# Kernel optimization log

Hardware: AMD Instinct MI355X
Metric: run time of the kernel (lower is better)

The kernel has to match this reference:

```python
import jax, jax.numpy as jnp
import numpy as np

N_ITERS = 3
EPS = 1e-5


def _ln(x, g, b):
    mu = jnp.mean(x, axis=-1, keepdims=True)
    var = jnp.mean((x - mu) ** 2, axis=-1, keepdims=True)
    return (x - mu) * jax.lax.rsqrt(var + EPS) * g + b


def setup_inputs() -> dict:
    key = jax.random.key(0)
    ks = iter(jax.random.split(key, 32))
    B, N, D_in, H, K = 128, 1024, 192, 128, 3

    def lin(o, i):
        w = (jax.random.normal(next(ks), (o, i)) / np.sqrt(i)).astype(jnp.float32)
        return w, jnp.zeros((o,), jnp.float32)

    Wp, bp = lin(H, D_in)
    Wq, bq = lin(H, H)
    Wk, bk = lin(H, H)
    Wv, bv = lin(H, H)
    Wih, bih = lin(3 * H, H)   # GRUCell input weights, stacked [r, z, n]
    Whh, bhh = lin(3 * H, H)   # GRUCell hidden weights
    W1, b1 = lin(2 * H, H)     # MLP expand
    W2, b2 = lin(H, 2 * H)     # MLP project
    ones = jnp.ones((H,), jnp.float32)
    zeros = jnp.zeros((H,), jnp.float32)

    return {
        "patch_tokens": jax.random.normal(next(ks), (B, N, D_in), jnp.float32),
        "noise": jax.random.normal(next(ks), (B, K, H), jnp.float32),
        "slot_mu": (jax.random.normal(next(ks), (1, K, H)) * 0.02).astype(jnp.float32),
        "slot_log_sigma": jnp.zeros((1, K, H), jnp.float32),
        "Wp": Wp, "bp": bp, "g_in": ones, "b_in": zeros,
        "Wq": Wq, "bq": bq, "Wk": Wk, "bk": bk, "Wv": Wv, "bv": bv,
        "Wih": Wih, "bih": bih, "Whh": Whh, "bhh": bhh,
        "g_s": ones, "b_s": zeros,
        "W1": W1, "b1": b1, "W2": W2, "b2": b2,
        "g_m": ones, "b_m": zeros,
    }


def reference(patch_tokens, noise, slot_mu, slot_log_sigma,
              Wp, bp, g_in, b_in,
              Wq, bq, Wk, bk, Wv, bv,
              Wih, bih, Whh, bhh,
              g_s, b_s, W1, b1, W2, b2, g_m, b_m):
    H = slot_mu.shape[-1]
    scale = 1.0 / jnp.sqrt(jnp.asarray(H, patch_tokens.dtype))

    # project + LayerNorm inputs once (k, v depend only on inputs -> hoisted)
    inputs = _ln(patch_tokens @ Wp.T + bp, g_in, b_in)      # (B, N, H)
    k = inputs @ Wk.T + bk                                  # (B, N, H)
    v = inputs @ Wv.T + bv                                  # (B, N, H)

    slots = slot_mu + jnp.exp(slot_log_sigma) * noise       # (B, K, H)

    def gru_cell(x, h):
        gi = x @ Wih.T + bih                                # (B, K, 3H)
        gh = h @ Whh.T + bhh
        ir, iz, inn = jnp.split(gi, 3, axis=-1)
        hr, hz, hn = jnp.split(gh, 3, axis=-1)
        r = jax.nn.sigmoid(ir + hr)
        z = jax.nn.sigmoid(iz + hz)
        n = jnp.tanh(inn + r * hn)
        return (1.0 - z) * n + z * h

    attn_weights = None
    for _ in range(N_ITERS):
        slots_prev = slots
        s = _ln(slots, g_s, b_s)
        q = s @ Wq.T + bq                                   # (B, K, H)
        attn = jnp.einsum('bkd,bnd->bkn', q, k) * scale     # (B, K, N)
        attn_weights = jax.nn.softmax(attn, axis=1)         # softmax over slots
        updates = jnp.einsum('bkn,bnd->bkd', attn_weights, v)
        slots = gru_cell(updates, slots_prev)
        h = _ln(slots, g_m, b_m)
        slots = slots + (jax.nn.gelu(h @ W1.T + b1, approximate=False) @ W2.T + b2)

    return slots, attn_weights
```

## Files before the change

### kernel.cpp

```cpp
#include <hip/hip_runtime.h>
#include <math.h>

constexpr float EPS = 1e-5f;
constexpr float SCALE = 0.08838834764831845f;

using f32x4  = __attribute__((ext_vector_type(4))) float;
using bf16x8 = __attribute__((ext_vector_type(8))) short;
using us8    = __attribute__((ext_vector_type(8))) unsigned short;

__device__ __forceinline__ unsigned short f2b_rne(float f) {
    unsigned int x = __float_as_uint(f);
    return (unsigned short)((x + 0x7fffu + ((x >> 16) & 1u)) >> 16);
}

__device__ __forceinline__ int swz32(int row, int k8) {
    int f = (row & 3) ^ ((row >> 2) & 3);
    return row * 32 + ((k8 ^ f) << 3);
}

__global__ __launch_bounds__(256) void split_weights_kernel(
    const float* __restrict__ Wp, const float* __restrict__ Wk,
    const float* __restrict__ Wv, unsigned short* __restrict__ hi,
    unsigned short* __restrict__ lo)
{
    int idx = blockIdx.x * 256 + threadIdx.x;
    float v;
    if (idx < 24576)      v = Wp[idx];
    else if (idx < 40960) v = Wk[idx - 24576];
    else                  v = Wv[idx - 40960];
    unsigned int bits = __float_as_uint(v);
    hi[idx] = (unsigned short)(bits >> 16);
    lo[idx] = f2b_rne(v - __uint_as_float(bits & 0xffff0000u));
}

__global__ __launch_bounds__(256) void pack_weights_kernel(
    const float* __restrict__ Wih, const float* __restrict__ Whh,
    const float* __restrict__ W1, const float* __restrict__ W2,
    const float* __restrict__ Wq, float4* __restrict__ out)
{
    int idx = blockIdx.x * 256 + threadIdx.x;
    const float* src; int OUT, base, K;
    if (idx < 12288)      { src = Wih; OUT = 384; base = 0;     K = 128; }
    else if (idx < 24576) { src = Whh; OUT = 384; base = 12288; K = 128; }
    else if (idx < 32768) { src = W1;  OUT = 256; base = 24576; K = 128; }
    else if (idx < 40960) { src = W2;  OUT = 128; base = 32768; K = 256; }
    else                  { src = Wq;  OUT = 128; base = 40960; K = 128; }
    int li = idx - base;
    int kq = li / OUT, t = li - kq * OUT;
    float4 v;
    v.x = src[(size_t)t * K + 4 * kq];
    v.y = src[(size_t)t * K + 4 * kq + 1];
    v.z = src[(size_t)t * K + 4 * kq + 2];
    v.w = src[(size_t)t * K + 4 * kq + 3];
    out[idx] = v;
}

__global__ __launch_bounds__(256, 3) void fused_proj_kv_kernel(
    const float* __restrict__ patch,
    const unsigned short* __restrict__ Wphi, const unsigned short* __restrict__ Wplo,
    const unsigned short* __restrict__ Wkhi, const unsigned short* __restrict__ Wklo,
    const unsigned short* __restrict__ Wvhi, const unsigned short* __restrict__ Wvlo,
    const float* __restrict__ biasp, const float* __restrict__ g_in,
    const float* __restrict__ b_in, const float* __restrict__ biask,
    const float* __restrict__ biasv,
    float* __restrict__ kout, float* __restrict__ vout)
{
    __shared__ __align__(16) unsigned short mem[24576];

    const int tid  = threadIdx.x;
    const int lane = tid & 63, wave = tid >> 6;
    const int ln15 = lane & 15, quad = lane >> 4;
    const int m0   = blockIdx.x * 64;

    const int wrow = wave * 16;
    f32x4 acc1[8];
#pragma unroll
    for (int nt = 0; nt < 8; nt++)
#pragma unroll
        for (int r = 0; r < 4; r++) acc1[nt][r] = 0.f;

    const int arow = tid >> 2, ak8 = tid & 3;
    const float* aptr = patch + (size_t)(m0 + arow) * 192 + ak8 * 8;
    float4 pa0 = *(const float4*)aptr;
    float4 pa1 = *(const float4*)(aptr + 4);
    us8 pbh[2], pbl[2];
    int boff[2];
#pragma unroll
    for (int i = 0; i < 2; i++) {
        int c = tid + 256 * i;
        boff[i] = (c >> 2) * 192 + (c & 3) * 8;
        pbh[i] = *(const us8*)(Wphi + boff[i]);
        pbl[i] = *(const us8*)(Wplo + boff[i]);
    }

    const int ea = swz32(wrow + ln15, quad);

    for (int kk = 0; kk < 192; kk += 32) {
        {
            float va[8] = {pa0.x, pa0.y, pa0.z, pa0.w, pa1.x, pa1.y, pa1.z, pa1.w};
            us8 h, l;
#pragma unroll
            for (int j = 0; j < 8; j++) {
                unsigned int bits = __float_as_uint(va[j]);
                h[j] = (unsigned short)(bits >> 16);
                l[j] = f2b_rne(va[j] - __uint_as_float(bits & 0xffff0000u));
            }
            int e = swz32(arow, ak8);
            *(us8*)&mem[e]        = h;
            *(us8*)&mem[2048 + e] = l;
        }
#pragma unroll
        for (int i = 0; i < 2; i++) {
            int c = tid + 256 * i;
            int e = swz32(c >> 2, c & 3);
            *(us8*)&mem[4096 + e] = pbh[i];
            *(us8*)&mem[8192 + e] = pbl[i];
        }
        __syncthreads();

        int kn = kk + 32;
        if (kn < 192) {
            pa0 = *(const float4*)(aptr + kn);
            pa1 = *(const float4*)(aptr + kn + 4);
#pragma unroll
            for (int i = 0; i < 2; i++) {
                pbh[i] = *(const us8*)(Wphi + boff[i] + kn);
                pbl[i] = *(const us8*)(Wplo + boff[i] + kn);
            }
        }

        bf16x8 ah = *(const bf16x8*)&mem[ea];
        bf16x8 al = *(const bf16x8*)&mem[2048 + ea];
#pragma unroll
        for (int nt = 0; nt < 8; nt++) {
            int eb = swz32(nt * 16 + ln15, quad);
            bf16x8 bh = *(const bf16x8*)&mem[4096 + eb];
            bf16x8 bl = *(const bf16x8*)&mem[8192 + eb];
            acc1[nt] = __builtin_amdgcn_mfma_f32_16x16x32_bf16(ah, bh, acc1[nt], 0, 0, 0);
            acc1[nt] = __builtin_amdgcn_mfma_f32_16x16x32_bf16(ah, bl, acc1[nt], 0, 0, 0);
            acc1[nt] = __builtin_amdgcn_mfma_f32_16x16x32_bf16(al, bh, acc1[nt], 0, 0, 0);
        }
        __syncthreads();
    }

    us8 pw[4];
#pragma unroll
    for (int i = 0; i < 4; i++) {
        const unsigned short* pl = (i >> 1) ? Wklo : Wkhi;
        int c = tid + (i & 1) * 256;
        pw[i] = *(const us8*)(pl + (size_t)(c >> 2) * 128 + (c & 3) * 8);
    }

    {
        float bb[8], gg[8], be[8];
#pragma unroll
        for (int nt = 0; nt < 8; nt++) {
            int col = nt * 16 + ln15;
            bb[nt] = biasp[col]; gg[nt] = g_in[col]; be[nt] = b_in[col];
        }
#pragma unroll
        for (int nt = 0; nt < 8; nt++)
#pragma unroll
            for (int r = 0; r < 4; r++) acc1[nt][r] += bb[nt];

        float mu[4], rs[4];
#pragma unroll
        for (int r = 0; r < 4; r++) {
            float s = 0.f, s2 = 0.f;
#pragma unroll
            for (int nt = 0; nt < 8; nt++) {
                float v = acc1[nt][r];
                s += v; s2 += v * v;
            }
#pragma unroll
            for (int off = 1; off < 16; off <<= 1) {
                s  += __shfl_xor(s,  off, 64);
                s2 += __shfl_xor(s2, off, 64);
            }
            float m = s * (1.f / 128.f);
            mu[r] = m;
            rs[r] = rsqrtf(s2 * (1.f / 128.f) - m * m + EPS);
        }
#pragma unroll
        for (int nt = 0; nt < 8; nt++)
#pragma unroll
            for (int r = 0; r < 4; r++) {
                float v = (acc1[nt][r] - mu[r]) * rs[r] * gg[nt] + be[nt];
                int row = wrow + quad * 4 + r, col = nt * 16 + ln15;
                int xi = (row * 128 + col) ^ ((row & 7) << 3);
                unsigned int bits = __float_as_uint(v);
                mem[xi]        = (unsigned short)(bits >> 16);
                mem[8192 + xi] = f2b_rne(v - __uint_as_float(bits & 0xffff0000u));
            }
    }

    const int R  = (wave & 1) * 32;
    const int Cb = (wave >> 1) * 64;
    const int xorx = (ln15 & 7) << 3;

    float bbk[4], bbv[4];
#pragma unroll
    for (int nt = 0; nt < 4; nt++) {
        int col = Cb + nt * 16 + ln15;
        bbk[nt] = biask[col];
        bbv[nt] = biasv[col];
    }

    f32x4 acc[2][4];
#pragma unroll
    for (int mt = 0; mt < 2; mt++)
#pragma unroll
        for (int nt = 0; nt < 4; nt++)
#pragma unroll
            for (int r = 0; r < 4; r++) acc[mt][nt][r] = 0.f;

    for (int s = 0; s < 8; s++) {
#pragma unroll
        for (int i = 0; i < 4; i++) {
            int c = tid + (i & 1) * 256;
            int e = 16384 + (i >> 1) * 4096 + swz32(c >> 2, c & 3);
            *(us8*)&mem[e] = pw[i];
        }
        __syncthreads();

        if (s < 7) {
            int sn = s + 1, kkn = (sn & 3) * 32;
            const unsigned short* ph = (sn >> 2) ? Wvhi : Wkhi;
            const unsigned short* po = (sn >> 2) ? Wvlo : Wklo;
#pragma unroll
            for (int i = 0; i < 4; i++) {
                const unsigned short* pl = (i >> 1) ? po : ph;
                int c = tid + (i & 1) * 256;
                pw[i] = *(const us8*)(pl + (size_t)(c >> 2) * 128 + (c & 3) * 8 + kkn);
            }
        }

        int kk = (s & 3) * 32;
        bf16x8 xh[2], xl[2];
#pragma unroll
        for (int mt = 0; mt < 2; mt++) {
            int row = R + mt * 16 + ln15;
            int ei = (row * 128 + kk + quad * 8) ^ xorx;
            xh[mt] = *(const bf16x8*)&mem[ei];
            xl[mt] = *(const bf16x8*)&mem[8192 + ei];
        }
#pragma unroll
        for (int nt = 0; nt < 4; nt++) {
            int eb = 16384 + swz32(Cb + nt * 16 + ln15, quad);
            bf16x8 wh = *(const bf16x8*)&mem[eb];
            bf16x8 wl = *(const bf16x8*)&mem[4096 + eb];
#pragma unroll
            for (int mt = 0; mt < 2; mt++) {
                acc[mt][nt] = __builtin_amdgcn_mfma_f32_16x16x32_bf16(xh[mt], wh, acc[mt][nt], 0, 0, 0);
                acc[mt][nt] = __builtin_amdgcn_mfma_f32_16x16x32_bf16(xh[mt], wl, acc[mt][nt], 0, 0, 0);
                acc[mt][nt] = __builtin_amdgcn_mfma_f32_16x16x32_bf16(xl[mt], wh, acc[mt][nt], 0, 0, 0);
            }
        }

        if (s == 3) {
#pragma unroll
            for (int mt = 0; mt < 2; mt++)
#pragma unroll
                for (int nt = 0; nt < 4; nt++)
#pragma unroll
                    for (int r = 0; r < 4; r++) {
                        size_t o = (size_t)(m0 + R + mt * 16 + quad * 4 + r) * 128
                                 + Cb + nt * 16 + ln15;
                        kout[o] = acc[mt][nt][r] + bbk[nt];
                        acc[mt][nt][r] = 0.f;
                    }
        }
        if (s < 7) __syncthreads();
    }

#pragma unroll
    for (int mt = 0; mt < 2; mt++)
#pragma unroll
        for (int nt = 0; nt < 4; nt++)
#pragma unroll
            for (int r = 0; r < 4; r++) {
                size_t o = (size_t)(m0 + R + mt * 16 + quad * 4 + r) * 128
                         + Cb + nt * 16 + ln15;
                vout[o] = acc[mt][nt][r] + bbv[nt];
            }
}

__global__ __launch_bounds__(128) void init_lnq_kernel(
    const float* __restrict__ noise, const float* __restrict__ smu,
    const float* __restrict__ sls, const float* __restrict__ g_s,
    const float* __restrict__ b_s, const float4* __restrict__ WqT4,
    const float* __restrict__ bq, float* __restrict__ slots,
    float* __restrict__ q)
{
    __shared__ float s_l[128];
    __shared__ float red[4];
    const int row = blockIdx.x, tid = threadIdx.x;
    const int k = row % 3;
    float x = smu[k * 128 + tid] + expf(sls[k * 128 + tid]) * noise[row * 128 + tid];
    slots[row * 128 + tid] = x;

    float s = x, s2 = x * x;
#pragma unroll
    for (int off = 32; off >= 1; off >>= 1) {
        s += __shfl_down(s, off, 64); s2 += __shfl_down(s2, off, 64);
    }
    if ((tid & 63) == 0) { red[tid >> 6] = s; red[2 + (tid >> 6)] = s2; }
    __syncthreads();
    float S = red[0] + red[1], S2 = red[2] + red[3];
    float m = S * (1.f / 128.f);
    float r = rsqrtf(S2 * (1.f / 128.f) - m * m + EPS);
    s_l[tid] = (x - m) * r * g_s[tid] + b_s[tid];
    __syncthreads();

    float a = bq[tid];
#pragma unroll 8
    for (int kq = 0; kq < 32; kq++) {
        float4 w = WqT4[kq * 128 + tid];
        a += s_l[4 * kq] * w.x + s_l[4 * kq + 1] * w.y
           + s_l[4 * kq + 2] * w.z + s_l[4 * kq + 3] * w.w;
    }
    q[row * 128 + tid] = a;
}

__global__ __launch_bounds__(256) void attn_kernel(
    const float* __restrict__ q, const float* __restrict__ kbuf,
    const float* __restrict__ vbuf, float* __restrict__ upd_part,
    float* __restrict__ attn_out, int write_attn)
{
    __shared__ float q_l[3][132];
    __shared__ __align__(16) float kv[64][132];
    __shared__ float lg[3][64];
    __shared__ float w_l[3][64];
    const int b = blockIdx.y, chunk = blockIdx.x, n0 = chunk * 64, tid = threadIdx.x;

    for (int idx = tid; idx < 384; idx += 256) {
        int s = idx >> 7, c = idx & 127;
        q_l[s][c + (c >> 5)] = q[b * 384 + idx];
    }
    const float4* vg = (const float4*)(vbuf + ((size_t)b * 1024 + n0) * 128);
    for (int idx = tid; idx < 2048; idx += 256) {
        int n = idx >> 5, c = (idx & 31) * 4;
        *(float4*)&kv[n][c] = vg[idx];
    }
    const int n = tid >> 2, q4 = tid & 3;
    float4 kr[8];
    const float4* kg4 = (const float4*)(kbuf + ((size_t)b * 1024 + n0 + n) * 128 + q4 * 32);
#pragma unroll
    for (int i = 0; i < 8; i++) kr[i] = kg4[i];
    __syncthreads();

    {
        const float* q0 = &q_l[0][q4 * 33];
        const float* q1 = &q_l[1][q4 * 33];
        const float* q2 = &q_l[2][q4 * 33];
        float p0 = 0.f, p1 = 0.f, p2 = 0.f;
#pragma unroll
        for (int i = 0; i < 8; i++) {
            float kx[4] = {kr[i].x, kr[i].y, kr[i].z, kr[i].w};
#pragma unroll
            for (int j = 0; j < 4; j++) {
                float vv = kx[j];
                p0 += q0[4 * i + j] * vv;
                p1 += q1[4 * i + j] * vv;
                p2 += q2[4 * i + j] * vv;
            }
        }
        p0 += __shfl_xor(p0, 1, 64); p0 += __shfl_xor(p0, 2, 64);
        p1 += __shfl_xor(p1, 1, 64); p1 += __shfl_xor(p1, 2, 64);
        p2 += __shfl_xor(p2, 1, 64); p2 += __shfl_xor(p2, 2, 64);
        if (q4 == 0) {
            lg[0][n] = p0 * SCALE; lg[1][n] = p1 * SCALE; lg[2][n] = p2 * SCALE;
        }
    }
    __syncthreads();

    if (tid < 64) {
        float l0 = lg[0][tid], l1 = lg[1][tid], l2 = lg[2][tid];
        float m = fmaxf(l0, fmaxf(l1, l2));
        float e0 = expf(l0 - m), e1 = expf(l1 - m), e2 = expf(l2 - m);
        float inv = 1.f / (e0 + e1 + e2);
        w_l[0][tid] = e0 * inv; w_l[1][tid] = e1 * inv; w_l[2][tid] = e2 * inv;
        if (write_attn) {
            attn_out[b * 3072 + n0 + tid]        = e0 * inv;
            attn_out[b * 3072 + 1024 + n0 + tid] = e1 * inv;
            attn_out[b * 3072 + 2048 + n0 + tid] = e2 * inv;
        }
    }
    __syncthreads();

    if (tid < 128) {
        float p0 = 0.f, p1 = 0.f, p2 = 0.f;
#pragma unroll 8
        for (int nn = 0; nn < 64; nn++) {
            float vv = kv[nn][tid];
            p0 += w_l[0][nn] * vv; p1 += w_l[1][nn] * vv; p2 += w_l[2][nn] * vv;
        }
        size_t base = (((size_t)b * 16 + chunk) * 3) * 128 + tid;
        upd_part[base]       = p0;
        upd_part[base + 128] = p1;
        upd_part[base + 256] = p2;
    }
}

__global__ __launch_bounds__(384) void gru_mlp_kernel(
    const float* __restrict__ slots_in, const float* __restrict__ upd_part,
    const float4* __restrict__ WihT4, const float* __restrict__ bih,
    const float4* __restrict__ WhhT4, const float* __restrict__ bhh,
    const float* __restrict__ g_m, const float* __restrict__ b_m,
    const float4* __restrict__ W1T4, const float* __restrict__ b1,
    const float4* __restrict__ W2T4, const float* __restrict__ b2,
    const float* __restrict__ g_s, const float* __restrict__ b_s,
    const float4* __restrict__ WqT4, const float* __restrict__ bq,
    float* __restrict__ slots_out, float* __restrict__ q_out, int write_q)
{
    __shared__ float u2[2][128];
    __shared__ float u_l[128], h_l[128];
    __shared__ float r_l[128], z_l[128], in_l[128], hn_l[128];
    __shared__ float n_l[128], hid_l[256], w2p[256];
    __shared__ float red[4];
    const int row = blockIdx.x, tid = threadIdx.x;
    const int bb_ = row / 3, ss = row - bb_ * 3;

    if (tid < 256) {
        int col = tid & 127, half = tid >> 7;
        const float* up = upd_part + (((size_t)bb_ * 16 + half * 8) * 3 + ss) * 128 + col;
        float u = 0.f;
#pragma unroll
        for (int c = 0; c < 8; c++) u += up[(size_t)c * 384];
        u2[half][col] = u;
        if (half == 0) h_l[col] = slots_in[row * 128 + col];
    }
    __syncthreads();
    if (tid < 128) u_l[tid] = u2[0][tid] + u2[1][tid];
    __syncthreads();

    {
        float gi = bih[tid], gh = bhh[tid];
#pragma unroll 8
        for (int kq = 0; kq < 32; kq++) {
            float4 a = WihT4[kq * 384 + tid];
            float4 c = WhhT4[kq * 384 + tid];
            gi += u_l[4 * kq] * a.x + u_l[4 * kq + 1] * a.y
                + u_l[4 * kq + 2] * a.z + u_l[4 * kq + 3] * a.w;
            gh += h_l[4 * kq] * c.x + h_l[4 * kq + 1] * c.y
                + h_l[4 * kq + 2] * c.z + h_l[4 * kq + 3] * c.w;
        }
        if (tid < 128)      r_l[tid] = 1.f / (1.f + expf(-(gi + gh)));
        else if (tid < 256) z_l[tid - 128] = 1.f / (1.f + expf(-(gi + gh)));
        else { in_l[tid - 256] = gi; hn_l[tid - 256] = gh; }
    }
    __syncthreads();

    float hnew = 0.f;
    if (tid < 128) {
        float nn = tanhf(in_l[tid] + r_l[tid] * hn_l[tid]);
        hnew = (1.f - z_l[tid]) * nn + z_l[tid] * h_l[tid];
        float s = hnew, s2 = hnew * hnew;
#pragma unroll
        for (int off = 32; off >= 1; off >>= 1) {
            s += __shfl_down(s, off, 64); s2 += __shfl_down(s2, off, 64);
        }
        if ((tid & 63) == 0) { red[tid >> 6] = s; red[2 + (tid >> 6)] = s2; }
    }
    __syncthreads();
    if (tid < 128) {
        float S = red[0] + red[1], S2 = red[2] + red[3];
        float m1 = S * (1.f / 128.f);
        float r1 = rsqrtf(S2 * (1.f / 128.f) - m1 * m1 + EPS);
        n_l[tid] = (hnew - m1) * r1 * g_m[tid] + b_m[tid];
    }
    __syncthreads();

    if (tid < 256) {
        float a = b1[tid];
#pragma unroll 8
        for (int kq = 0; kq < 32; kq++) {
            float4 w = W1T4[kq * 256 + tid];
            a += n_l[4 * kq] * w.x + n_l[4 * kq + 1] * w.y
               + n_l[4 * kq + 2] * w.z + n_l[4 * kq + 3] * w.w;
        }
        a = 0.5f * a * (1.f + erff(a * 0.70710678118654752f));
        hid_l[tid] = a;
    }
    __syncthreads();

    if (tid < 256) {
        int out = tid & 127, half = tid >> 7;
        float p = 0.f;
#pragma unroll 8
        for (int kq = half * 32; kq < half * 32 + 32; kq++) {
            float4 w = W2T4[kq * 128 + out];
            p += hid_l[4 * kq] * w.x + hid_l[4 * kq + 1] * w.y
               + hid_l[4 * kq + 2] * w.z + hid_l[4 * kq + 3] * w.w;
        }
        w2p[tid] = p;
    }
    __syncthreads();

    float snew = 0.f;
    if (tid < 128) {
        snew = hnew + b2[tid] + (w2p[tid] + w2p[128 + tid]);
        slots_out[row * 128 + tid] = snew;
    }

    if (write_q) {
        if (tid < 128) {
            float t1 = snew, t2 = snew * snew;
#pragma unroll
            for (int off = 32; off >= 1; off >>= 1) {
                t1 += __shfl_down(t1, off, 64); t2 += __shfl_down(t2, off, 64);
            }
            if ((tid & 63) == 0) { red[tid >> 6] = t1; red[2 + (tid >> 6)] = t2; }
        }
        __syncthreads();
        if (tid < 128) {
            float T = red[0] + red[1], T2 = red[2] + red[3];
            float m2 = T * (1.f / 128.f);
            float r2 = rsqrtf(T2 * (1.f / 128.f) - m2 * m2 + EPS);
            n_l[tid] = (snew - m2) * r2 * g_s[tid] + b_s[tid];
        }
        __syncthreads();
        if (tid < 256) {
            int out = tid & 127, half = tid >> 7;
            float p = (half == 0) ? bq[out] : 0.f;
#pragma unroll 8
            for (int kq = half * 16; kq < half * 16 + 16; kq++) {
                float4 w = WqT4[kq * 128 + out];
                p += n_l[4 * kq] * w.x + n_l[4 * kq + 1] * w.y
                   + n_l[4 * kq + 2] * w.z + n_l[4 * kq + 3] * w.w;
            }
            w2p[tid] = p;
        }
        __syncthreads();
        if (tid < 128) q_out[row * 128 + tid] = w2p[tid] + w2p[128 + tid];
    }
}

extern "C" void kernel_launch(void* const* d_in, const int* in_sizes, int n_in,
                              void* d_out, int out_size, void* d_ws, size_t ws_size,
                              hipStream_t stream)
{
    const float* patch   = (const float*)d_in[0];
    const float* noise   = (const float*)d_in[1];
    const float* slot_mu = (const float*)d_in[2];
    const float* slot_ls = (const float*)d_in[3];
    const float* Wp = (const float*)d_in[4];  const float* bp = (const float*)d_in[5];
    const float* g_in = (const float*)d_in[6]; const float* b_in = (const float*)d_in[7];
    const float* Wq = (const float*)d_in[8];  const float* bq = (const float*)d_in[9];
    const float* Wk = (const float*)d_in[10]; const float* bk = (const float*)d_in[11];
    const float* Wv = (const float*)d_in[12]; const float* bv = (const float*)d_in[13];
    const float* Wih = (const float*)d_in[14]; const float* bih = (const float*)d_in[15];
    const float* Whh = (const float*)d_in[16]; const float* bhh = (const float*)d_in[17];
    const float* g_s = (const float*)d_in[18]; const float* b_s = (const float*)d_in[19];
    const float* W1 = (const float*)d_in[20]; const float* b1 = (const float*)d_in[21];
    const float* W2 = (const float*)d_in[22]; const float* b2 = (const float*)d_in[23];
    const float* g_m = (const float*)d_in[24]; const float* b_m = (const float*)d_in[25];

    float* kbuf = (float*)d_ws;
    float* vbuf = kbuf + 16777216;
    unsigned short* w_hi = (unsigned short*)(vbuf + 16777216);
    unsigned short* w_lo = w_hi + 57344;
    unsigned short* wp_hi = w_hi,        * wp_lo = w_lo;
    unsigned short* wk_hi = w_hi + 24576,* wk_lo = w_lo + 24576;
    unsigned short* wv_hi = w_hi + 40960,* wv_lo = w_lo + 40960;
    float4* wt4 = (float4*)(w_lo + 57344);
    float4* wihT4 = wt4;
    float4* whhT4 = wt4 + 12288;
    float4* w1T4  = wt4 + 24576;
    float4* w2T4  = wt4 + 32768;
    float4* wqT4  = wt4 + 40960;
    float* slots = (float*)(wt4 + 45056);
    float* qbuf  = slots + 49152;
    float* part  = qbuf + 49152;

    float* out_slots = (float*)d_out;
    float* out_attn  = (float*)d_out + 49152;

    split_weights_kernel<<<224, 256, 0, stream>>>(Wp, Wk, Wv, w_hi, w_lo);
    pack_weights_kernel<<<176, 256, 0, stream>>>(Wih, Whh, W1, W2, Wq, wt4);

    fused_proj_kv_kernel<<<2048, 256, 0, stream>>>(
        patch, wp_hi, wp_lo, wk_hi, wk_lo, wv_hi, wv_lo,
        bp, g_in, b_in, bk, bv, kbuf, vbuf);

    init_lnq_kernel<<<384, 128, 0, stream>>>(noise, slot_mu, slot_ls,
                                             g_s, b_s, wqT4, bq, slots, qbuf);

    for (int it = 0; it < 3; it++) {
        attn_kernel<<<dim3(16, 128), 256, 0, stream>>>(
            qbuf, kbuf, vbuf, part, out_attn, it == 2 ? 1 : 0);
        gru_mlp_kernel<<<384, 384, 0, stream>>>(
            slots, part, wihT4, bih, whhT4, bhh, g_m, b_m, w1T4, b1, w2T4, b2,
            g_s, b_s, wqT4, bq,
            (it == 2) ? out_slots : slots, qbuf, it == 2 ? 0 : 1);
    }
}
```

Measured before the change: 379.5 us.

## Fuse all slot-attention iterations into one persistent per-batch kernel

Replaces init_lnq plus the three attn/gru_mlp launch pairs with a single slot_iter_kernel. It runs one 512-thread block per batch element, keeps slots, q and partial updates in shared memory, and double-buffers K/V chunks in registers. It also merges the two weight-prep kernels into one launch and preloads all patch rows up front in the projection kernel. This removes about seven launches and the global round-trips of q, slots and partial sums. The cost is that only 128 blocks run, each streaming its batch's full K/V serially three times, so the GPU may be underfilled and bandwidth-bound per CU.

After: 753.1 us. 98.5% more time.

```diff
diff --git a/kernel.cpp b/kernel.cpp
--- a/kernel.cpp
+++ b/kernel.cpp
@@ -18,41 +18,40 @@
     return row * 32 + ((k8 ^ f) << 3);
 }
 
-__global__ __launch_bounds__(256) void split_weights_kernel(
+__global__ __launch_bounds__(256) void prep_weights_kernel(
     const float* __restrict__ Wp, const float* __restrict__ Wk,
-    const float* __restrict__ Wv, unsigned short* __restrict__ hi,
-    unsigned short* __restrict__ lo)
+    const float* __restrict__ Wv, const float* __restrict__ Wih,
+    const float* __restrict__ Whh, const float* __restrict__ W1,
+    const float* __restrict__ W2, const float* __restrict__ Wq,
+    unsigned short* __restrict__ hi, unsigned short* __restrict__ lo,
+    float4* __restrict__ wt4)
 {
     int idx = blockIdx.x * 256 + threadIdx.x;
-    float v;
-    if (idx < 24576)      v = Wp[idx];
-    else if (idx < 40960) v = Wk[idx - 24576];
-    else                  v = Wv[idx - 40960];
-    unsigned int bits = __float_as_uint(v);
-    hi[idx] = (unsigned short)(bits >> 16);
-    lo[idx] = f2b_rne(v - __uint_as_float(bits & 0xffff0000u));
-}
-
-__global__ __launch_bounds__(256) void pack_weights_kernel(
-    const float* __restrict__ Wih, const float* __restrict__ Whh,
-    const float* __restrict__ W1, const float* __restrict__ W2,
-    const float* __restrict__ Wq, float4* __restrict__ out)
-{
-    int idx = blockIdx.x * 256 + threadIdx.x;
-    const float* src; int OUT, base, K;
-    if (idx < 12288)      { src = Wih; OUT = 384; base = 0;     K = 128; }
-    else if (idx < 24576) { src = Whh; OUT = 384; base = 12288; K = 128; }
-    else if (idx < 32768) { src = W1;  OUT = 256; base = 24576; K = 128; }
-    else if (idx < 40960) { src = W2;  OUT = 128; base = 32768; K = 256; }
-    else                  { src = Wq;  OUT = 128; base = 40960; K = 128; }
-    int li = idx - base;
-    int kq = li / OUT, t = li - kq * OUT;
-    float4 v;
-    v.x = src[(size_t)t * K + 4 * kq];
-    v.y = src[(size_t)t * K + 4 * kq + 1];
-    v.z = src[(size_t)t * K + 4 * kq + 2];
-    v.w = src[(size_t)t * K + 4 * kq + 3];
-    out[idx] = v;
+    if (idx < 57344) {
+        float v;
+        if (idx < 24576)      v = Wp[idx];
+        else if (idx < 40960) v = Wk[idx - 24576];
+        else                  v = Wv[idx - 40960];
+        unsigned int bits = __float_as_uint(v);
+        hi[idx] = (unsigned short)(bits >> 16);
+        lo[idx] = f2b_rne(v - __uint_as_float(bits & 0xffff0000u));
+    } else {
+        int li = idx - 57344;
+        const float* src; int OUT, base, K;
+        if (li < 12288)      { src = Wih; OUT = 384; base = 0;     K = 128; }
+        else if (li < 24576) { src = Whh; OUT = 384; base = 12288; K = 128; }
+        else if (li < 32768) { src = W1;  OUT = 256; base = 24576; K = 128; }
+        else if (li < 40960) { src = W2;  OUT = 128; base = 32768; K = 256; }
+        else                 { src = Wq;  OUT = 128; base = 40960; K = 128; }
+        int lo2 = li - base;
+        int kq = lo2 / OUT, t = lo2 - kq * OUT;
+        float4 v;
+        v.x = src[(size_t)t * K + 4 * kq];
+        v.y = src[(size_t)t * K + 4 * kq + 1];
+        v.z = src[(size_t)t * K + 4 * kq + 2];
+        v.w = src[(size_t)t * K + 4 * kq + 3];
+        wt4[li] = v;
+    }
 }
 
 __global__ __launch_bounds__(256, 3) void fused_proj_kv_kernel(
@@ -81,8 +80,12 @@
 
     const int arow = tid >> 2, ak8 = tid & 3;
     const float* aptr = patch + (size_t)(m0 + arow) * 192 + ak8 * 8;
-    float4 pa0 = *(const float4*)aptr;
-    float4 pa1 = *(const float4*)(aptr + 4);
+    float4 pa[6][2];
+#pragma unroll
+    for (int t6 = 0; t6 < 6; t6++) {
+        pa[t6][0] = *(const float4*)(aptr + t6 * 32);
+        pa[t6][1] = *(const float4*)(aptr + t6 * 32 + 4);
+    }
     us8 pbh[2], pbl[2];
     int boff[2];
 #pragma unroll
@@ -95,9 +98,11 @@
 
     const int ea = swz32(wrow + ln15, quad);
 
-    for (int kk = 0; kk < 192; kk += 32) {
+#pragma unroll
+    for (int st = 0; st < 6; st++) {
         {
-            float va[8] = {pa0.x, pa0.y, pa0.z, pa0.w, pa1.x, pa1.y, pa1.z, pa1.w};
+            float va[8] = {pa[st][0].x, pa[st][0].y, pa[st][0].z, pa[st][0].w,
+                           pa[st][1].x, pa[st][1].y, pa[st][1].z, pa[st][1].w};
             us8 h, l;
 #pragma unroll
             for (int j = 0; j < 8; j++) {
@@ -118,10 +123,8 @@
         }
         __syncthreads();
 
-        int kn = kk + 32;
-        if (kn < 192) {
-            pa0 = *(const float4*)(aptr + kn);
-            pa1 = *(const float4*)(aptr + kn + 4);
+        if (st < 5) {
+            int kn = (st + 1) * 32;
 #pragma unroll
             for (int i = 0; i < 2; i++) {
                 pbh[i] = *(const us8*)(Wphi + boff[i] + kn);
@@ -214,6 +217,7 @@
 #pragma unroll
             for (int r = 0; r < 4; r++) acc[mt][nt][r] = 0.f;
 
+#pragma unroll
     for (int s = 0; s < 8; s++) {
 #pragma unroll
         for (int i = 0; i < 4; i++) {
@@ -285,254 +289,298 @@
             }
 }
 
-__global__ __launch_bounds__(128) void init_lnq_kernel(
+__global__ __launch_bounds__(512, 1) void slot_iter_kernel(
     const float* __restrict__ noise, const float* __restrict__ smu,
-    const float* __restrict__ sls, const float* __restrict__ g_s,
-    const float* __restrict__ b_s, const float4* __restrict__ WqT4,
-    const float* __restrict__ bq, float* __restrict__ slots,
-    float* __restrict__ q)
-{
-    __shared__ float s_l[128];
-    __shared__ float red[4];
-    const int row = blockIdx.x, tid = threadIdx.x;
-    const int k = row % 3;
-    float x = smu[k * 128 + tid] + expf(sls[k * 128 + tid]) * noise[row * 128 + tid];
-    slots[row * 128 + tid] = x;
-
-    float s = x, s2 = x * x;
-#pragma unroll
-    for (int off = 32; off >= 1; off >>= 1) {
-        s += __shfl_down(s, off, 64); s2 += __shfl_down(s2, off, 64);
-    }
-    if ((tid & 63) == 0) { red[tid >> 6] = s; red[2 + (tid >> 6)] = s2; }
-    __syncthreads();
-    float S = red[0] + red[1], S2 = red[2] + red[3];
-    float m = S * (1.f / 128.f);
-    float r = rsqrtf(S2 * (1.f / 128.f) - m * m + EPS);
-    s_l[tid] = (x - m) * r * g_s[tid] + b_s[tid];
-    __syncthreads();
-
-    float a = bq[tid];
-#pragma unroll 8
-    for (int kq = 0; kq < 32; kq++) {
-        float4 w = WqT4[kq * 128 + tid];
-        a += s_l[4 * kq] * w.x + s_l[4 * kq + 1] * w.y
-           + s_l[4 * kq + 2] * w.z + s_l[4 * kq + 3] * w.w;
-    }
-    q[row * 128 + tid] = a;
-}
-
-__global__ __launch_bounds__(256) void attn_kernel(
-    const float* __restrict__ q, const float* __restrict__ kbuf,
-    const float* __restrict__ vbuf, float* __restrict__ upd_part,
-    float* __restrict__ attn_out, int write_attn)
-{
-    __shared__ float q_l[3][132];
-    __shared__ __align__(16) float kv[64][132];
-    __shared__ float lg[3][64];
-    __shared__ float w_l[3][64];
-    const int b = blockIdx.y, chunk = blockIdx.x, n0 = chunk * 64, tid = threadIdx.x;
-
-    for (int idx = tid; idx < 384; idx += 256) {
-        int s = idx >> 7, c = idx & 127;
-        q_l[s][c + (c >> 5)] = q[b * 384 + idx];
-    }
-    const float4* vg = (const float4*)(vbuf + ((size_t)b * 1024 + n0) * 128);
-    for (int idx = tid; idx < 2048; idx += 256) {
-        int n = idx >> 5, c = (idx & 31) * 4;
-        *(float4*)&kv[n][c] = vg[idx];
-    }
-    const int n = tid >> 2, q4 = tid & 3;
-    float4 kr[8];
-    const float4* kg4 = (const float4*)(kbuf + ((size_t)b * 1024 + n0 + n) * 128 + q4 * 32);
-#pragma unroll
-    for (int i = 0; i < 8; i++) kr[i] = kg4[i];
-    __syncthreads();
-
-    {
-        const float* q0 = &q_l[0][q4 * 33];
-        const float* q1 = &q_l[1][q4 * 33];
-        const float* q2 = &q_l[2][q4 * 33];
-        float p0 = 0.f, p1 = 0.f, p2 = 0.f;
-#pragma unroll
-        for (int i = 0; i < 8; i++) {
-            float kx[4] = {kr[i].x, kr[i].y, kr[i].z, kr[i].w};
-#pragma unroll
-            for (int j = 0; j < 4; j++) {
-                float vv = kx[j];
-                p0 += q0[4 * i + j] * vv;
-                p1 += q1[4 * i + j] * vv;
-                p2 += q2[4 * i + j] * vv;
-            }
-        }
-        p0 += __shfl_xor(p0, 1, 64); p0 += __shfl_xor(p0, 2, 64);
-        p1 += __shfl_xor(p1, 1, 64); p1 += __shfl_xor(p1, 2, 64);
-        p2 += __shfl_xor(p2, 1, 64); p2 += __shfl_xor(p2, 2, 64);
-        if (q4 == 0) {
-            lg[0][n] = p0 * SCALE; lg[1][n] = p1 * SCALE; lg[2][n] = p2 * SCALE;
-        }
-    }
-    __syncthreads();
-
-    if (tid < 64) {
-        float l0 = lg[0][tid], l1 = lg[1][tid], l2 = lg[2][tid];
-        float m = fmaxf(l0, fmaxf(l1, l2));
-        float e0 = expf(l0 - m), e1 = expf(l1 - m), e2 = expf(l2 - m);
-        float inv = 1.f / (e0 + e1 + e2);
-        w_l[0][tid] = e0 * inv; w_l[1][tid] = e1 * inv; w_l[2][tid] = e2 * inv;
-        if (write_attn) {
-            attn_out[b * 3072 + n0 + tid]        = e0 * inv;
-            attn_out[b * 3072 + 1024 + n0 + tid] = e1 * inv;
-            attn_out[b * 3072 + 2048 + n0 + tid] = e2 * inv;
-        }
-    }
-    __syncthreads();
-
-    if (tid < 128) {
-        float p0 = 0.f, p1 = 0.f, p2 = 0.f;
-#pragma unroll 8
-        for (int nn = 0; nn < 64; nn++) {
-            float vv = kv[nn][tid];
-            p0 += w_l[0][nn] * vv; p1 += w_l[1][nn] * vv; p2 += w_l[2][nn] * vv;
-        }
-        size_t base = (((size_t)b * 16 + chunk) * 3) * 128 + tid;
-        upd_part[base]       = p0;
-        upd_part[base + 128] = p1;
-        upd_part[base + 256] = p2;
-    }
-}
-
-__global__ __launch_bounds__(384) void gru_mlp_kernel(
-    const float* __restrict__ slots_in, const float* __restrict__ upd_part,
+    const float* __restrict__ sls,
+    const float* __restrict__ g_s, const float* __restrict__ b_s,
+    const float4* __restrict__ WqT4, const float* __restrict__ bq,
+    const float* __restrict__ kbuf, const float* __restrict__ vbuf,
     const float4* __restrict__ WihT4, const float* __restrict__ bih,
     const float4* __restrict__ WhhT4, const float* __restrict__ bhh,
     const float* __restrict__ g_m, const float* __restrict__ b_m,
     const float4* __restrict__ W1T4, const float* __restrict__ b1,
     const float4* __restrict__ W2T4, const float* __restrict__ b2,
-    const float* __restrict__ g_s, const float* __restrict__ b_s,
-    const float4* __restrict__ WqT4, const float* __restrict__ bq,
-    float* __restrict__ slots_out, float* __restrict__ q_out, int write_q)
+    float* __restrict__ out_slots, float* __restrict__ out_attn)
 {
-    __shared__ float u2[2][128];
-    __shared__ float u_l[128], h_l[128];
-    __shared__ float r_l[128], z_l[128], in_l[128], hn_l[128];
-    __shared__ float n_l[128], hid_l[256], w2p[256];
-    __shared__ float red[4];
-    const int row = blockIdx.x, tid = threadIdx.x;
-    const int bb_ = row / 3, ss = row - bb_ * 3;
-
-    if (tid < 256) {
-        int col = tid & 127, half = tid >> 7;
-        const float* up = upd_part + (((size_t)bb_ * 16 + half * 8) * 3 + ss) * 128 + col;
-        float u = 0.f;
-#pragma unroll
-        for (int c = 0; c < 8; c++) u += up[(size_t)c * 384];
-        u2[half][col] = u;
-        if (half == 0) h_l[col] = slots_in[row * 128 + col];
+    __shared__ float q_l[3][132];
+    __shared__ float h_l[3][128];
+    __shared__ float u_l[3][128];
+    __shared__ float hn2[3][128];
+    __shared__ float n_l[3][128];
+    __shared__ float r_l[3][128], z_l[3][128], in_l[3][128], hnl[3][128];
+    __shared__ float part[16][3][128];
+    __shared__ float lg[3][128], w_l[3][128];
+    __shared__ float hid_l[3][256];
+    __shared__ float w2p[2][3][128];
+    __shared__ float red[3][4];
+
+    const int b = blockIdx.x, tid = threadIdx.x;
+
+    const float* kb_ = kbuf + (size_t)b * 131072;
+    const float* vb_ = vbuf + (size_t)b * 131072;
+    const float4* kp4 = (const float4*)(kb_ + (size_t)(tid >> 2) * 128 + (tid & 3) * 32);
+    const float* vp = vb_ + (size_t)(tid >> 5) * 1024 + (tid & 31) * 4;
+
+    if (tid < 384) {
+        int s = tid >> 7, d = tid & 127;
+        float x = smu[s * 128 + d] + expf(sls[s * 128 + d]) * noise[(size_t)b * 384 + tid];
+        h_l[s][d] = x;
     }
     __syncthreads();
-    if (tid < 128) u_l[tid] = u2[0][tid] + u2[1][tid];
-    __syncthreads();
-
-    {
-        float gi = bih[tid], gh = bhh[tid];
-#pragma unroll 8
-        for (int kq = 0; kq < 32; kq++) {
-            float4 a = WihT4[kq * 384 + tid];
-            float4 c = WhhT4[kq * 384 + tid];
-            gi += u_l[4 * kq] * a.x + u_l[4 * kq + 1] * a.y
-                + u_l[4 * kq + 2] * a.z + u_l[4 * kq + 3] * a.w;
-            gh += h_l[4 * kq] * c.x + h_l[4 * kq + 1] * c.y
-                + h_l[4 * kq + 2] * c.z + h_l[4 * kq + 3] * c.w;
-        }
-        if (tid < 128)      r_l[tid] = 1.f / (1.f + expf(-(gi + gh)));
-        else if (tid < 256) z_l[tid - 128] = 1.f / (1.f + expf(-(gi + gh)));
-        else { in_l[tid - 256] = gi; hn_l[tid - 256] = gh; }
-    }
-    __syncthreads();
-
-    float hnew = 0.f;
-    if (tid < 128) {
-        float nn = tanhf(in_l[tid] + r_l[tid] * hn_l[tid]);
-        hnew = (1.f - z_l[tid]) * nn + z_l[tid] * h_l[tid];
-        float s = hnew, s2 = hnew * hnew;
-#pragma unroll
-        for (int off = 32; off >= 1; off >>= 1) {
-            s += __shfl_down(s, off, 64); s2 += __shfl_down(s2, off, 64);
-        }
-        if ((tid & 63) == 0) { red[tid >> 6] = s; red[2 + (tid >> 6)] = s2; }
-    }
-    __syncthreads();
-    if (tid < 128) {
-        float S = red[0] + red[1], S2 = red[2] + red[3];
-        float m1 = S * (1.f / 128.f);
-        float r1 = rsqrtf(S2 * (1.f / 128.f) - m1 * m1 + EPS);
-        n_l[tid] = (hnew - m1) * r1 * g_m[tid] + b_m[tid];
-    }
-    __syncthreads();
-
-    if (tid < 256) {
-        float a = b1[tid];
-#pragma unroll 8
-        for (int kq = 0; kq < 32; kq++) {
-            float4 w = W1T4[kq * 256 + tid];
-            a += n_l[4 * kq] * w.x + n_l[4 * kq + 1] * w.y
-               + n_l[4 * kq + 2] * w.z + n_l[4 * kq + 3] * w.w;
-        }
-        a = 0.5f * a * (1.f + erff(a * 0.70710678118654752f));
-        hid_l[tid] = a;
-    }
-    __syncthreads();
-
-    if (tid < 256) {
-        int out = tid & 127, half = tid >> 7;
-        float p = 0.f;
-#pragma unroll 8
-        for (int kq = half * 32; kq < half * 32 + 32; kq++) {
-            float4 w = W2T4[kq * 128 + out];
-            p += hid_l[4 * kq] * w.x + hid_l[4 * kq + 1] * w.y
-               + hid_l[4 * kq + 2] * w.z + hid_l[4 * kq + 3] * w.w;
-        }
-        w2p[tid] = p;
-    }
-    __syncthreads();
-
-    float snew = 0.f;
-    if (tid < 128) {
-        snew = hnew + b2[tid] + (w2p[tid] + w2p[128 + tid]);
-        slots_out[row * 128 + tid] = snew;
-    }
-
-    if (write_q) {
+
+    float4 ka[8], kb2[8], va[8], vb2[8];
+    float4 acc0, acc1, acc2;
+
+    auto attn_chunk = [&](int c, float4 (&kc)[8], float4 (&vc)[8],
+                          float4 (&kn)[8], float4 (&vn)[8], bool pf, bool wout) {
+        if (pf) {
+            const float4* kpn = kp4 + (c + 1) * 4096;
+            const float* vpn = vp + (c + 1) * 16384;
+#pragma unroll
+            for (int i = 0; i < 8; i++) kn[i] = kpn[i];
+#pragma unroll
+            for (int j = 0; j < 8; j++) vn[j] = *(const float4*)(vpn + j * 128);
+        }
+        {
+            const float* q0 = &q_l[0][(tid & 3) * 33];
+            const float* q1 = &q_l[1][(tid & 3) * 33];
+            const float* q2 = &q_l[2][(tid & 3) * 33];
+            float p0 = 0.f, p1 = 0.f, p2 = 0.f;
+#pragma unroll
+            for (int i = 0; i < 8; i++) {
+                float kx[4] = {kc[i].x, kc[i].y, kc[i].z, kc[i].w};
+#pragma unroll
+                for (int j = 0; j < 4; j++) {
+                    float vv = kx[j];
+                    p0 += q0[4 * i + j] * vv;
+                    p1 += q1[4 * i + j] * vv;
+                    p2 += q2[4 * i + j] * vv;
+                }
+            }
+            p0 += __shfl_xor(p0, 1, 64); p0 += __shfl_xor(p0, 2, 64);
+            p1 += __shfl_xor(p1, 1, 64); p1 += __shfl_xor(p1, 2, 64);
+            p2 += __shfl_xor(p2, 1, 64); p2 += __shfl_xor(p2, 2, 64);
+            if ((tid & 3) == 0) {
+                int n = tid >> 2;
+                lg[0][n] = p0 * SCALE; lg[1][n] = p1 * SCALE; lg[2][n] = p2 * SCALE;
+            }
+        }
+        __syncthreads();
         if (tid < 128) {
-            float t1 = snew, t2 = snew * snew;
-#pragma unroll
-            for (int off = 32; off >= 1; off >>= 1) {
-                t1 += __shfl_down(t1, off, 64); t2 += __shfl_down(t2, off, 64);
-            }
-            if ((tid & 63) == 0) { red[tid >> 6] = t1; red[2 + (tid >> 6)] = t2; }
-        }
-        __syncthreads();
-        if (tid < 128) {
-            float T = red[0] + red[1], T2 = red[2] + red[3];
-            float m2 = T * (1.f / 128.f);
-            float r2 = rsqrtf(T2 * (1.f / 128.f) - m2 * m2 + EPS);
-            n_l[tid] = (snew - m2) * r2 * g_s[tid] + b_s[tid];
+            float l0 = lg[0][tid], l1 = lg[1][tid], l2 = lg[2][tid];
+            float m = fmaxf(l0, fmaxf(l1, l2));
+            float e0 = expf(l0 - m), e1 = expf(l1 - m), e2 = expf(l2 - m);
+            float inv = 1.f / (e0 + e1 + e2);
+            w_l[0][tid] = e0 * inv; w_l[1][tid] = e1 * inv; w_l[2][tid] = e2 * inv;
+            if (wout) {
+                int n = c * 128 + tid;
+                out_attn[b * 3072 + n]        = e0 * inv;
+                out_attn[b * 3072 + 1024 + n] = e1 * inv;
+                out_attn[b * 3072 + 2048 + n] = e2 * inv;
+            }
+        }
+        __syncthreads();
+        {
+            int tg = tid >> 5;
+#pragma unroll
+            for (int j = 0; j < 8; j++) {
+                float w0 = w_l[0][tg * 8 + j];
+                float w1 = w_l[1][tg * 8 + j];
+                float w2 = w_l[2][tg * 8 + j];
+                float4 vv = vc[j];
+                acc0.x += w0 * vv.x; acc0.y += w0 * vv.y; acc0.z += w0 * vv.z; acc0.w += w0 * vv.w;
+                acc1.x += w1 * vv.x; acc1.y += w1 * vv.y; acc1.z += w1 * vv.z; acc1.w += w1 * vv.w;
+                acc2.x += w2 * vv.x; acc2.y += w2 * vv.y; acc2.z += w2 * vv.z; acc2.w += w2 * vv.w;
+            }
+        }
+        __syncthreads();
+    };
+
+    for (int it = 0; it < 3; ++it) {
+        const bool last = (it == 2);
+
+#pragma unroll
+        for (int i = 0; i < 8; i++) ka[i] = kp4[i];
+#pragma unroll
+        for (int j = 0; j < 8; j++) va[j] = *(const float4*)(vp + j * 128);
+
+        if (tid < 384) {
+            int s = tid >> 7;
+            float x = h_l[s][tid & 127];
+            float s1 = x, s2 = x * x;
+#pragma unroll
+            for (int off = 1; off < 64; off <<= 1) {
+                s1 += __shfl_xor(s1, off, 64); s2 += __shfl_xor(s2, off, 64);
+            }
+            if ((tid & 63) == 0) {
+                int wv = (tid >> 6) & 1;
+                red[s][wv] = s1; red[s][2 + wv] = s2;
+            }
+        }
+        __syncthreads();
+        if (tid < 384) {
+            int s = tid >> 7, d = tid & 127;
+            float S = red[s][0] + red[s][1], S2 = red[s][2] + red[s][3];
+            float m = S * (1.f / 128.f);
+            float r = rsqrtf(S2 * (1.f / 128.f) - m * m + EPS);
+            n_l[s][d] = (h_l[s][d] - m) * r * g_s[d] + b_s[d];
         }
         __syncthreads();
         if (tid < 256) {
             int out = tid & 127, half = tid >> 7;
-            float p = (half == 0) ? bq[out] : 0.f;
-#pragma unroll 8
+            float p0 = half ? 0.f : bq[out], p1 = p0, p2 = p0;
+#pragma unroll
             for (int kq = half * 16; kq < half * 16 + 16; kq++) {
                 float4 w = WqT4[kq * 128 + out];
-                p += n_l[4 * kq] * w.x + n_l[4 * kq + 1] * w.y
-                   + n_l[4 * kq + 2] * w.z + n_l[4 * kq + 3] * w.w;
-            }
-            w2p[tid] = p;
-        }
-        __syncthreads();
-        if (tid < 128) q_out[row * 128 + tid] = w2p[tid] + w2p[128 + tid];
+                p0 += n_l[0][4 * kq] * w.x + n_l[0][4 * kq + 1] * w.y
+                    + n_l[0][4 * kq + 2] * w.z + n_l[0][4 * kq + 3] * w.w;
+                p1 += n_l[1][4 * kq] * w.x + n_l[1][4 * kq + 1] * w.y
+                    + n_l[1][4 * kq + 2] * w.z + n_l[1][4 * kq + 3] * w.w;
+                p2 += n_l[2][4 * kq] * w.x + n_l[2][4 * kq + 1] * w.y
+                    + n_l[2][4 * kq + 2] * w.z + n_l[2][4 * kq + 3] * w.w;
+            }
+            w2p[half][0][out] = p0; w2p[half][1][out] = p1; w2p[half][2][out] = p2;
+        }
+        __syncthreads();
+        if (tid < 384) {
+            int s = tid >> 7, d = tid & 127;
+            float qv = w2p[0][s][d] + w2p[1][s][d];
+            q_l[s][d + (d >> 5)] = qv;
+        }
+        __syncthreads();
+
+        acc0 = {0.f, 0.f, 0.f, 0.f}; acc1 = acc0; acc2 = acc0;
+        attn_chunk(0, ka, va, kb2, vb2, true, last);
+        attn_chunk(1, kb2, vb2, ka, va, true, last);
+        attn_chunk(2, ka, va, kb2, vb2, true, last);
+        attn_chunk(3, kb2, vb2, ka, va, true, last);
+        attn_chunk(4, ka, va, kb2, vb2, true, last);
+        attn_chunk(5, kb2, vb2, ka, va, true, last);
+        attn_chunk(6, ka, va, kb2, vb2, true, last);
+        attn_chunk(7, kb2, vb2, ka, va, false, last);
+
+        {
+            int tg = tid >> 5, d0 = (tid & 31) * 4;
+            *(float4*)&part[tg][0][d0] = acc0;
+            *(float4*)&part[tg][1][d0] = acc1;
+            *(float4*)&part[tg][2][d0] = acc2;
+        }
+        __syncthreads();
+        if (tid < 384) {
+            int s = tid >> 7, d = tid & 127;
+            float u = 0.f;
+#pragma unroll
+            for (int tg = 0; tg < 16; tg++) u += part[tg][s][d];
+            u_l[s][d] = u;
+        }
+        __syncthreads();
+
+        if (tid < 384) {
+            float gi0 = bih[tid], gi1 = gi0, gi2 = gi0;
+            float gh0 = bhh[tid], gh1 = gh0, gh2 = gh0;
+#pragma unroll 8
+            for (int kq = 0; kq < 32; kq++) {
+                float4 a = WihT4[kq * 384 + tid];
+                float4 c4 = WhhT4[kq * 384 + tid];
+                gi0 += u_l[0][4 * kq] * a.x + u_l[0][4 * kq + 1] * a.y
+                     + u_l[0][4 * kq + 2] * a.z + u_l[0][4 * kq + 3] * a.w;
+                gi1 += u_l[1][4 * kq] * a.x + u_l[1][4 * kq + 1] * a.y
+                     + u_l[1][4 * kq + 2] * a.z + u_l[1][4 * kq + 3] * a.w;
+                gi2 += u_l[2][4 * kq] * a.x + u_l[2][4 * kq + 1] * a.y
+                     + u_l[2][4 * kq + 2] * a.z + u_l[2][4 * kq + 3] * a.w;
+                gh0 += h_l[0][4 * kq] * c4.x + h_l[0][4 * kq + 1] * c4.y
+                     + h_l[0][4 * kq + 2] * c4.z + h_l[0][4 * kq + 3] * c4.w;
+                gh1 += h_l[1][4 * kq] * c4.x + h_l[1][4 * kq + 1] * c4.y
+                     + h_l[1][4 * kq + 2] * c4.z + h_l[1][4 * kq + 3] * c4.w;
+                gh2 += h_l[2][4 * kq] * c4.x + h_l[2][4 * kq + 1] * c4.y
+                     + h_l[2][4 * kq + 2] * c4.z + h_l[2][4 * kq + 3] * c4.w;
+            }
+            if (tid < 128) {
+                r_l[0][tid] = 1.f / (1.f + expf(-(gi0 + gh0)));
+                r_l[1][tid] = 1.f / (1.f + expf(-(gi1 + gh1)));
+                r_l[2][tid] = 1.f / (1.f + expf(-(gi2 + gh2)));
+            } else if (tid < 256) {
+                int d = tid - 128;
+                z_l[0][d] = 1.f / (1.f + expf(-(gi0 + gh0)));
+                z_l[1][d] = 1.f / (1.f + expf(-(gi1 + gh1)));
+                z_l[2][d] = 1.f / (1.f + expf(-(gi2 + gh2)));
+            } else {
+                int d = tid - 256;
+                in_l[0][d] = gi0; hnl[0][d] = gh0;
+                in_l[1][d] = gi1; hnl[1][d] = gh1;
+                in_l[2][d] = gi2; hnl[2][d] = gh2;
+            }
+        }
+        __syncthreads();
+
+        if (tid < 384) {
+            int s = tid >> 7, d = tid & 127;
+            float nn = tanhf(in_l[s][d] + r_l[s][d] * hnl[s][d]);
+            float hnewv = (1.f - z_l[s][d]) * nn + z_l[s][d] * h_l[s][d];
+            hn2[s][d] = hnewv;
+            float s1 = hnewv, s2 = hnewv * hnewv;
+#pragma unroll
+            for (int off = 1; off < 64; off <<= 1) {
+                s1 += __shfl_xor(s1, off, 64); s2 += __shfl_xor(s2, off, 64);
+            }
+            if ((tid & 63) == 0) {
+                int wv = (tid >> 6) & 1;
+                red[s][wv] = s1; red[s][2 + wv] = s2;
+            }
+        }
+        __syncthreads();
+        if (tid < 384) {
+            int s = tid >> 7, d = tid & 127;
+            float S = red[s][0] + red[s][1], S2 = red[s][2] + red[s][3];
+            float m1 = S * (1.f / 128.f);
+            float r1 = rsqrtf(S2 * (1.f / 128.f) - m1 * m1 + EPS);
+            n_l[s][d] = (hn2[s][d] - m1) * r1 * g_m[d] + b_m[d];
+        }
+        __syncthreads();
+
+        if (tid < 256) {
+            float a0 = b1[tid], a1 = a0, a2 = a0;
+#pragma unroll 8
+            for (int kq = 0; kq < 32; kq++) {
+                float4 w = W1T4[kq * 256 + tid];
+                a0 += n_l[0][4 * kq] * w.x + n_l[0][4 * kq + 1] * w.y
+                    + n_l[0][4 * kq + 2] * w.z + n_l[0][4 * kq + 3] * w.w;
+                a1 += n_l[1][4 * kq] * w.x + n_l[1][4 * kq + 1] * w.y
+                    + n_l[1][4 * kq + 2] * w.z + n_l[1][4 * kq + 3] * w.w;
+                a2 += n_l[2][4 * kq] * w.x + n_l[2][4 * kq + 1] * w.y
+                    + n_l[2][4 * kq + 2] * w.z + n_l[2][4 * kq + 3] * w.w;
+            }
+            a0 = 0.5f * a0 * (1.f + erff(a0 * 0.70710678118654752f));
+            a1 = 0.5f * a1 * (1.f + erff(a1 * 0.70710678118654752f));
+            a2 = 0.5f * a2 * (1.f + erff(a2 * 0.70710678118654752f));
+            hid_l[0][tid] = a0; hid_l[1][tid] = a1; hid_l[2][tid] = a2;
+        }
+        __syncthreads();
+
+        if (tid < 256) {
+            int out = tid & 127, half = tid >> 7;
+            float p0 = 0.f, p1 = 0.f, p2 = 0.f;
+#pragma unroll 8
+            for (int kq = half * 32; kq < half * 32 + 32; kq++) {
+                float4 w = W2T4[kq * 128 + out];
+                p0 += hid_l[0][4 * kq] * w.x + hid_l[0][4 * kq + 1] * w.y
+                    + hid_l[0][4 * kq + 2] * w.z + hid_l[0][4 * kq + 3] * w.w;
+                p1 += hid_l[1][4 * kq] * w.x + hid_l[1][4 * kq + 1] * w.y
+                    + hid_l[1][4 * kq + 2] * w.z + hid_l[1][4 * kq + 3] * w.w;
+                p2 += hid_l[2][4 * kq] * w.x + hid_l[2][4 * kq + 1] * w.y
+                    + hid_l[2][4 * kq + 2] * w.z + hid_l[2][4 * kq + 3] * w.w;
+            }
+            w2p[half][0][out] = p0; w2p[half][1][out] = p1; w2p[half][2][out] = p2;
+        }
+        __syncthreads();
+
+        if (tid < 384) {
+            int s = tid >> 7, d = tid & 127;
+            float snew = hn2[s][d] + b2[d] + w2p[0][s][d] + w2p[1][s][d];
+            h_l[s][d] = snew;
+            if (last) out_slots[b * 384 + tid] = snew;
+        }
+        __syncthreads();
     }
 }
 
@@ -569,29 +617,19 @@
     float4* w1T4  = wt4 + 24576;
     float4* w2T4  = wt4 + 32768;
     float4* wqT4  = wt4 + 40960;
-    float* slots = (float*)(wt4 + 45056);
-    float* qbuf  = slots + 49152;
-    float* part  = qbuf + 49152;
 
     float* out_slots = (float*)d_out;
     float* out_attn  = (float*)d_out + 49152;
 
-    split_weights_kernel<<<224, 256, 0, stream>>>(Wp, Wk, Wv, w_hi, w_lo);
-    pack_weights_kernel<<<176, 256, 0, stream>>>(Wih, Whh, W1, W2, Wq, wt4);
+    prep_weights_kernel<<<400, 256, 0, stream>>>(
+        Wp, Wk, Wv, Wih, Whh, W1, W2, Wq, w_hi, w_lo, wt4);
 
     fused_proj_kv_kernel<<<2048, 256, 0, stream>>>(
         patch, wp_hi, wp_lo, wk_hi, wk_lo, wv_hi, wv_lo,
         bp, g_in, b_in, bk, bv, kbuf, vbuf);
 
-    init_lnq_kernel<<<384, 128, 0, stream>>>(noise, slot_mu, slot_ls,
-                                             g_s, b_s, wqT4, bq, slots, qbuf);
-
-    for (int it = 0; it < 3; it++) {
-        attn_kernel<<<dim3(16, 128), 256, 0, stream>>>(
-            qbuf, kbuf, vbuf, part, out_attn, it == 2 ? 1 : 0);
-        gru_mlp_kernel<<<384, 384, 0, stream>>>(
-            slots, part, wihT4, bih, whhT4, bhh, g_m, b_m, w1T4, b1, w2T4, b2,
-            g_s, b_s, wqT4, bq,
-            (it == 2) ? out_slots : slots, qbuf, it == 2 ? 0 : 1);
-    }
+    slot_iter_kernel<<<128, 512, 0, stream>>>(
+        noise, slot_mu, slot_ls, g_s, b_s, wqT4, bq, kbuf, vbuf,
+        wihT4, bih, whhT4, bhh, g_m, b_m, w1T4, b1, w2T4, b2,
+        out_slots, out_attn);
 }
```
